# Optimization experiments

Hardware: AMD Instinct MI355X
Metric: run time of the kernel (lower is better)

The kernel has to match this reference:

```python
import jax, jax.numpy as jnp
import numpy as np

B = 64          # batch
IN_CH = 128     # in_channels
OUT_CH = 128    # out_channels
MODES = 64      # modes1
N = 4096        # spatial length (power of two -> pad branches in original are no-ops)


def _fht1d(x):
    """Faithful vectorized version of the recursive fht1d.

    x: (M, n) with n a power of two. Same DIT recursion as the torch code:
    X = [E + cas*O, E - cas*O], cas(theta) = cos(theta) + sin(theta).
    Even/odd halves are stacked along the leading axis so the recursion is
    traced only log2(n) times (fully vectorized at each level).
    """
    n = x.shape[-1]
    if n == 1:
        return x
    sub = _fht1d(jnp.concatenate([x[:, 0::2], x[:, 1::2]], axis=0))  # (2M, n/2)
    e, o = jnp.split(sub, 2, axis=0)
    k = jnp.arange(n // 2, dtype=x.dtype)
    theta = (2.0 * jnp.pi / n) * k
    cas = jnp.cos(theta) + jnp.sin(theta)
    t = cas * o
    return jnp.concatenate([e + t, e - t], axis=-1)


def dht_last(x):
    """DHT along the last dim of x (B, C, N); N is a power of two."""
    shp = x.shape
    return _fht1d(x.reshape(-1, shp[-1])).reshape(shp)


def compl_mul1d(x1, x2):
    # x1: (b, i, m), x2: (i, o, m); Hartley-domain "complex" multiply.
    neg = lambda a: jnp.roll(jnp.flip(a, axis=-1), 1, axis=-1)  # H(-k)
    x1n = neg(x1)
    x2n = neg(x2)
    return 0.5 * (
        jnp.einsum('bix,iox->box', x1, x2)
        - jnp.einsum('bix,iox->box', x1n, x2n)
        + jnp.einsum('bix,iox->box', x1, x2n)
        + jnp.einsum('bix,iox->box', x1n, x2)
    )


def setup_inputs() -> dict:
    key = jax.random.key(0)
    kx, kw = jax.random.split(key)
    x = jax.random.normal(kx, (B, IN_CH, N), dtype=jnp.float32)
    scale = 1.0 / (IN_CH * OUT_CH)
    weights1 = scale * jax.random.uniform(kw, (IN_CH, OUT_CH, MODES), dtype=jnp.float32)
    return {"x": x, "weights1": weights1}


def reference(x, weights1):
    n = x.shape[-1]
    modes = weights1.shape[-1]
    x_ht = dht_last(x)                                  # (B, IN_CH, N)
    mixed = compl_mul1d(x_ht[:, :, :modes], weights1)   # (B, OUT_CH, modes)
    out_ht = jnp.zeros((x.shape[0], weights1.shape[1], n), dtype=x.dtype)
    out_ht = out_ht.at[:, :, :modes].set(mixed)
    # idht = dht / N
    return dht_last(out_ht) / n
```

## Files before the change

### kernel.cpp

```cpp
#include <hip/hip_runtime.h>
#include <math.h>

#define PI2F 6.28318530717958647692f

__host__ __device__ constexpr int br6(int p) {
    return ((p & 1) << 5) | ((p & 2) << 3) | ((p & 4) << 1) |
           ((p & 8) >> 1) | ((p & 16) >> 3) | ((p & 32) >> 5);
}
__host__ __device__ constexpr int brN(int v, int bits) {
    int r = 0;
    for (int i = 0; i < bits; ++i) r |= ((v >> i) & 1) << (bits - 1 - i);
    return r;
}

__device__ static constexpr float CAS8T[4] = {1.f, 1.41421356f, 1.f, 0.f};
__device__ static constexpr float CAS16T[8] = {
    1.f, 1.30656296f, 1.41421356f, 1.30656296f, 1.f, 0.54119610f, 0.f, -0.54119610f};
__device__ static constexpr float CAS32T[16] = {
    1.f, 1.17587560f, 1.30656296f, 1.38703985f, 1.41421356f, 1.38703985f,
    1.30656296f, 1.17587560f, 1.f, 0.78569496f, 0.54119610f, 0.27589938f,
    0.f, -0.27589938f, -0.54119610f, -0.78569496f};
__device__ static constexpr float CAS64T[32] = {
    1.f, 1.09320187f, 1.17587560f, 1.24722502f, 1.30656296f, 1.35331800f,
    1.38703985f, 1.40740373f, 1.41421356f, 1.40740373f, 1.38703985f,
    1.35331800f, 1.30656296f, 1.24722502f, 1.17587560f, 1.09320187f,
    1.f, 0.89716759f, 0.78569496f, 0.66665566f, 0.54119610f, 0.41052452f,
    0.27589938f, 0.13861717f, 0.f, -0.13861717f, -0.27589938f, -0.41052452f,
    -0.54119610f, -0.66665566f, -0.78569496f, -0.89716759f};

__global__ __launch_bounds__(256) void wtrans_cast(const float* __restrict__ w,
                                                   float* __restrict__ wp,
                                                   float* __restrict__ wm,
                                                   float* __restrict__ casT) {
    const int tid = threadIdx.x;
    if (blockIdx.x == 128) {
        if (blockIdx.y != 0) return;
#pragma unroll
        for (int base = 0; base < 4096; base += 256) {
            const int idx = base + tid;
            if (idx < 4032) {
                const int j = idx >> 6, r = idx & 63;
                int l, u;
                if (j == 0) { l = 5; u = 0; }
                else if (j < 3) { l = 4; u = j - 1; }
                else if (j < 7) { l = 3; u = j - 3; }
                else if (j < 15) { l = 2; u = j - 7; }
                else if (j < 31) { l = 1; u = j - 15; }
                else { l = 0; u = j - 31; }
                float s, c;
                sincosf(PI2F * (float)(r + 64 * u) / (float)(4096 >> l), &s, &c);
                casT[j * 64 + r] = c + s;
            }
        }
        return;
    }
    __shared__ float W[64 * 65];
    const int i = blockIdx.x;
    const int oh = blockIdx.y;
    const float* src = w + (size_t)i * 8192 + oh * 4096;
#pragma unroll
    for (int it = 0; it < 4; ++it) {
        const int k = it * 1024 + tid * 4;
        const float4 v = *(const float4*)(src + k);
        const int ol = k >> 6;
        const int ml = k & 63;
        W[ol * 65 + ml + 0] = v.x;
        W[ol * 65 + ml + 1] = v.y;
        W[ol * 65 + ml + 2] = v.z;
        W[ol * 65 + ml + 3] = v.w;
    }
    __syncthreads();
    const int mh = tid >> 6;
    const int ol = tid & 63;
    const int o = oh * 64 + ol;
#pragma unroll
    for (int ml = 0; ml < 16; ++ml) {
        const int m = mh * 16 + ml;
        const int mp = (64 - m) & 63;
        const float a = W[ol * 65 + m];
        const float b = W[ol * 65 + mp];
        wp[((size_t)m * 128 + i) * 128 + o] = 0.5f * (a + b);
        wm[((size_t)m * 128 + i) * 128 + o] = 0.5f * (a - b);
    }
}

__global__ __launch_bounds__(64) void fht_fwd(const float* __restrict__ x,
                                              float* __restrict__ xh_t) {
    __shared__ float Y[64 * 65];
    const int lane = threadIdx.x;

    float a6[6];
#pragma unroll
    for (int l = 0; l < 6; ++l) {
        float s, c;
        sincosf(PI2F * (float)lane / (float)(4096 >> l), &s, &c);
        a6[l] = c + s;
    }
    float G[64];
    G[0] = 1.0f;
#pragma unroll
    for (int c = 1; c < 64; ++c) G[c] = G[c & (c - 1)] * a6[__builtin_ctz(c)];

    const int row0 = blockIdx.x * 2;
    float accs[2];
#pragma unroll 1
    for (int rr = 0; rr < 2; ++rr) {
        const float* xr = x + (size_t)(row0 + rr) * 4096;
#pragma unroll
        for (int j = 0; j < 16; ++j) {
            const float4 v4 = *(const float4*)(xr + (j * 64 + lane) * 4);
            *(float4*)&Y[(j * 64 + lane) * 4] = v4;
        }
        __syncthreads();
        float v[64];
#pragma unroll
        for (int p = 0; p < 64; ++p) v[p] = Y[64 * br6(p) + lane];
        __syncthreads();

#pragma unroll
        for (int b = 0; b < 64; b += 2) {
            float t0 = v[b], t1 = v[b + 1];
            v[b] = t0 + t1; v[b + 1] = t0 - t1;
        }
#pragma unroll
        for (int b = 0; b < 64; b += 4)
#pragma unroll
            for (int k = 0; k < 2; ++k) {
                float t0 = v[b + k], t1 = v[b + k + 2];
                v[b + k] = t0 + t1; v[b + k + 2] = t0 - t1;
            }
#pragma unroll
        for (int b = 0; b < 64; b += 8)
#pragma unroll
            for (int k = 0; k < 4; ++k) {
                float w = CAS8T[k];
                float t0 = v[b + k], t1 = v[b + k + 4];
                v[b + k] = fmaf(w, t1, t0); v[b + k + 4] = fmaf(-w, t1, t0);
            }
#pragma unroll
        for (int b = 0; b < 64; b += 16)
#pragma unroll
            for (int k = 0; k < 8; ++k) {
                float w = CAS16T[k];
                float t0 = v[b + k], t1 = v[b + k + 8];
                v[b + k] = fmaf(w, t1, t0); v[b + k + 8] = fmaf(-w, t1, t0);
            }
#pragma unroll
        for (int b = 0; b < 64; b += 32)
#pragma unroll
            for (int k = 0; k < 16; ++k) {
                float w = CAS32T[k];
                float t0 = v[b + k], t1 = v[b + k + 16];
                v[b + k] = fmaf(w, t1, t0); v[b + k + 16] = fmaf(-w, t1, t0);
            }
#pragma unroll
        for (int k = 0; k < 32; ++k) {
            float w = CAS64T[k];
            float t0 = v[k], t1 = v[k + 32];
            v[k] = fmaf(w, t1, t0); v[k + 32] = fmaf(-w, t1, t0);
        }

#pragma unroll
        for (int m = 0; m < 64; ++m) Y[lane * 65 + m] = v[m];
        __syncthreads();
        float acc = 0.0f;
#pragma unroll
        for (int c = 0; c < 64; ++c) acc = fmaf(G[c], Y[c * 65 + lane], acc);
        __syncthreads();
        accs[rr] = acc;
    }
    *(float2*)(xh_t + (size_t)lane * 8192 + row0) = make_float2(accs[0], accs[1]);
}

__global__ __launch_bounds__(256) void passB(const float* __restrict__ xh_t,
                                             const float* __restrict__ wp,
                                             const float* __restrict__ wm,
                                             float* __restrict__ mixed_t) {
    __shared__ float Us[8][132];
    __shared__ float Uns[8][132];
    const int tid = threadIdx.x;
    const int m = blockIdx.y;
    const int bt = blockIdx.x;
    const int mp = (64 - m) & 63;
    {
        const int bl = tid >> 5;
        const int i0 = (tid & 31) * 4;
        const float4 vu = *(const float4*)(xh_t + (size_t)m  * 8192 + bt * 1024 + tid * 4);
        const float4 vn = *(const float4*)(xh_t + (size_t)mp * 8192 + bt * 1024 + tid * 4);
        *(float4*)&Us[bl][i0] = vu;
        *(float4*)&Uns[bl][i0] = vn;
    }
    __syncthreads();
    const int b = tid >> 5;
    const int o0 = (tid & 31) * 4;
    float acc[4];
#pragma unroll
    for (int j = 0; j < 4; ++j) acc[j] = 0.0f;
#pragma unroll 4
    for (int i = 0; i < 128; ++i) {
        float p[4], q[4];
        *(float4*)&p[0] = *(const float4*)(wp + ((size_t)m * 128 + i) * 128 + o0);
        *(float4*)&q[0] = *(const float4*)(wm + ((size_t)m * 128 + i) * 128 + o0);
        const float u = Us[b][i];
        const float un = Uns[b][i];
#pragma unroll
        for (int j = 0; j < 4; ++j) acc[j] += u * p[j] + un * q[j];
    }
    float* dst = mixed_t + (size_t)m * 8192 + (bt * 8 + b) * 128 + o0;
    *(float4*)dst = make_float4(acc[0], acc[1], acc[2], acc[3]);
}

__global__ __launch_bounds__(64) void fht_inv(const float* __restrict__ mixed_t,
                                              const float* __restrict__ casT,
                                              float* __restrict__ out) {
    __shared__ float OS[4096];
    __shared__ __align__(16) float S[64];
    const int lane = threadIdx.x;
    float K[63];
#pragma unroll
    for (int j = 0; j < 63; ++j) K[j] = casT[j * 64 + lane];

    const int row0 = blockIdx.x * 4;
    float4 mv4 = *(const float4*)(mixed_t + (size_t)lane * 8192 + row0);
    mv4.x *= (1.0f / 4096.0f); mv4.y *= (1.0f / 4096.0f);
    mv4.z *= (1.0f / 4096.0f); mv4.w *= (1.0f / 4096.0f);
    float mvs[4] = {mv4.x, mv4.y, mv4.z, mv4.w};

#pragma unroll 1
    for (int rr = 0; rr < 4; ++rr) {
        const int row = row0 + rr;
        __syncthreads();
        S[lane] = mvs[rr];
        __syncthreads();
        float e[64];
#pragma unroll
        for (int m4 = 0; m4 < 16; ++m4) {
            const float4 q = *(const float4*)&S[4 * m4];
            e[4 * m4 + 0] = q.x; e[4 * m4 + 1] = q.y;
            e[4 * m4 + 2] = q.z; e[4 * m4 + 3] = q.w;
        }
#pragma unroll
        for (int mp = 0; mp < 32; ++mp) {
            float w = K[0];
            float t0 = e[mp], t1 = e[mp + 32];
            e[mp] = fmaf(w, t1, t0); e[mp + 32] = fmaf(-w, t1, t0);
        }
#pragma unroll
        for (int hi = 0; hi < 2; ++hi)
#pragma unroll
            for (int mp = 0; mp < 16; ++mp) {
                float w = K[1 + brN(hi, 1)];
                int i0 = hi * 32 + mp;
                float t0 = e[i0], t1 = e[i0 + 16];
                e[i0] = fmaf(w, t1, t0); e[i0 + 16] = fmaf(-w, t1, t0);
            }
#pragma unroll
        for (int hi = 0; hi < 4; ++hi)
#pragma unroll
            for (int mp = 0; mp < 8; ++mp) {
                float w = K[3 + brN(hi, 2)];
                int i0 = hi * 16 + mp;
                float t0 = e[i0], t1 = e[i0 + 8];
                e[i0] = fmaf(w, t1, t0); e[i0 + 8] = fmaf(-w, t1, t0);
            }
#pragma unroll
        for (int hi = 0; hi < 8; ++hi)
#pragma unroll
            for (int mp = 0; mp < 4; ++mp) {
                float w = K[7 + brN(hi, 3)];
                int i0 = hi * 8 + mp;
                float t0 = e[i0], t1 = e[i0 + 4];
                e[i0] = fmaf(w, t1, t0); e[i0 + 4] = fmaf(-w, t1, t0);
            }
#pragma unroll
        for (int hi = 0; hi < 16; ++hi)
#pragma unroll
            for (int mp = 0; mp < 2; ++mp) {
                float w = K[15 + brN(hi, 4)];
                int i0 = hi * 4 + mp;
                float t0 = e[i0], t1 = e[i0 + 2];
                e[i0] = fmaf(w, t1, t0); e[i0 + 2] = fmaf(-w, t1, t0);
            }
#pragma unroll
        for (int hi = 0; hi < 32; ++hi) {
            float w = K[31 + brN(hi, 5)];
            int i0 = hi * 2;
            float t0 = e[i0], t1 = e[i0 + 1];
            e[i0] = fmaf(w, t1, t0); e[i0 + 1] = fmaf(-w, t1, t0);
        }
#pragma unroll
        for (int t = 0; t < 64; ++t) OS[64 * t + lane] = e[br6(t)];
        __syncthreads();
        float* outr = out + (size_t)row * 4096;
#pragma unroll
        for (int j = 0; j < 16; ++j) {
            *(float4*)(outr + (j * 64 + lane) * 4) = *(const float4*)&OS[(j * 64 + lane) * 4];
        }
    }
}

extern "C" void kernel_launch(void* const* d_in, const int* in_sizes, int n_in,
                              void* d_out, int out_size, void* d_ws, size_t ws_size,
                              hipStream_t stream) {
    const float* x = (const float*)d_in[0];
    const float* w = (const float*)d_in[1];
    float* out = (float*)d_out;
    float* wsf = (float*)d_ws;

    float* casT    = wsf + 512;
    float* xh_t    = wsf + 8192;
    float* wp      = wsf + 532480;
    float* wm      = wsf + 1581056;
    float* mixed_t = wsf + 2629632;

    wtrans_cast<<<dim3(129, 2), dim3(256), 0, stream>>>(w, wp, wm, casT);
    fht_fwd<<<dim3(4096), dim3(64), 0, stream>>>(x, xh_t);
    passB<<<dim3(8, 64), dim3(256), 0, stream>>>(xh_t, wp, wm, mixed_t);
    fht_inv<<<dim3(2048), dim3(64), 0, stream>>>(mixed_t, casT, out);
}
```

Before: 268.1 us.

## Load and store FHT rows directly from global memory, factor twiddle accumulation

The forward FHT now reads input straight from global memory in bit-reversed strided order instead of staging through shared memory. The final cas-weighted reduction uses a log-depth factored FMA tree in place of a precomputed 64-entry G table, with a float4-padded shared transpose. The inverse FHT writes output directly with coalesced per-lane stores instead of going through a 16KB shared buffer. The passB grid dimensions are also swapped so m varies fastest. This reduces LDS usage and syncs, which may raise occupancy, at the cost of relying on caches for the strided loads.

```diff
diff --git a/kernel.cpp b/kernel.cpp
--- a/kernel.cpp
+++ b/kernel.cpp
@@ -86,7 +86,7 @@
 
 __global__ __launch_bounds__(64) void fht_fwd(const float* __restrict__ x,
                                               float* __restrict__ xh_t) {
-    __shared__ float Y[64 * 65];
+    __shared__ __align__(16) float Y[64 * 68];
     const int lane = threadIdx.x;
 
     float a6[6];
@@ -96,26 +96,15 @@
         sincosf(PI2F * (float)lane / (float)(4096 >> l), &s, &c);
         a6[l] = c + s;
     }
-    float G[64];
-    G[0] = 1.0f;
-#pragma unroll
-    for (int c = 1; c < 64; ++c) G[c] = G[c & (c - 1)] * a6[__builtin_ctz(c)];
 
     const int row0 = blockIdx.x * 2;
     float accs[2];
 #pragma unroll 1
     for (int rr = 0; rr < 2; ++rr) {
-        const float* xr = x + (size_t)(row0 + rr) * 4096;
-#pragma unroll
-        for (int j = 0; j < 16; ++j) {
-            const float4 v4 = *(const float4*)(xr + (j * 64 + lane) * 4);
-            *(float4*)&Y[(j * 64 + lane) * 4] = v4;
-        }
-        __syncthreads();
+        const float* xr = x + (size_t)(row0 + rr) * 4096 + lane;
         float v[64];
 #pragma unroll
-        for (int p = 0; p < 64; ++p) v[p] = Y[64 * br6(p) + lane];
-        __syncthreads();
+        for (int p = 0; p < 64; ++p) v[p] = xr[64 * br6(p)];
 
 #pragma unroll
         for (int b = 0; b < 64; b += 2) {
@@ -160,14 +149,22 @@
             v[k] = fmaf(w, t1, t0); v[k + 32] = fmaf(-w, t1, t0);
         }
 
-#pragma unroll
-        for (int m = 0; m < 64; ++m) Y[lane * 65 + m] = v[m];
         __syncthreads();
-        float acc = 0.0f;
-#pragma unroll
-        for (int c = 0; c < 64; ++c) acc = fmaf(G[c], Y[c * 65 + lane], acc);
+#pragma unroll
+        for (int m4 = 0; m4 < 16; ++m4)
+            *(float4*)&Y[lane * 68 + 4 * m4] =
+                make_float4(v[4 * m4], v[4 * m4 + 1], v[4 * m4 + 2], v[4 * m4 + 3]);
         __syncthreads();
-        accs[rr] = acc;
+#pragma unroll
+        for (int c = 0; c < 64; ++c) v[c] = Y[c * 68 + lane];
+#pragma unroll
+        for (int l = 0; l < 6; ++l) {
+            const int st = 1 << l;
+#pragma unroll
+            for (int k = 0; k < 64; k += 2 * st)
+                v[k] = fmaf(a6[l], v[k + st], v[k]);
+        }
+        accs[rr] = v[0];
     }
     *(float2*)(xh_t + (size_t)lane * 8192 + row0) = make_float2(accs[0], accs[1]);
 }
@@ -179,8 +176,8 @@
     __shared__ float Us[8][132];
     __shared__ float Uns[8][132];
     const int tid = threadIdx.x;
-    const int m = blockIdx.y;
-    const int bt = blockIdx.x;
+    const int m = blockIdx.x;
+    const int bt = blockIdx.y;
     const int mp = (64 - m) & 63;
     {
         const int bl = tid >> 5;
@@ -213,7 +210,6 @@
 __global__ __launch_bounds__(64) void fht_inv(const float* __restrict__ mixed_t,
                                               const float* __restrict__ casT,
                                               float* __restrict__ out) {
-    __shared__ float OS[4096];
     __shared__ __align__(16) float S[64];
     const int lane = threadIdx.x;
     float K[63];
@@ -288,14 +284,9 @@
             float t0 = e[i0], t1 = e[i0 + 1];
             e[i0] = fmaf(w, t1, t0); e[i0 + 1] = fmaf(-w, t1, t0);
         }
-#pragma unroll
-        for (int t = 0; t < 64; ++t) OS[64 * t + lane] = e[br6(t)];
-        __syncthreads();
-        float* outr = out + (size_t)row * 4096;
-#pragma unroll
-        for (int j = 0; j < 16; ++j) {
-            *(float4*)(outr + (j * 64 + lane) * 4) = *(const float4*)&OS[(j * 64 + lane) * 4];
-        }
+        float* outr = out + (size_t)row * 4096 + lane;
+#pragma unroll
+        for (int t = 0; t < 64; ++t) outr[64 * t] = e[br6(t)];
     }
 }
 
@@ -315,6 +306,6 @@
 
     wtrans_cast<<<dim3(129, 2), dim3(256), 0, stream>>>(w, wp, wm, casT);
     fht_fwd<<<dim3(4096), dim3(64), 0, stream>>>(x, xh_t);
-    passB<<<dim3(8, 64), dim3(256), 0, stream>>>(xh_t, wp, wm, mixed_t);
+    passB<<<dim3(64, 8), dim3(256), 0, stream>>>(xh_t, wp, wm, mixed_t);
     fht_inv<<<dim3(2048), dim3(64), 0, stream>>>(mixed_t, casT, out);
 }
```

Result: no change. 266.1 us (median of 2 runs) (-0.7%).
